# Kernel tuning notes

Hardware: AMD Instinct MI355X
Metric: run time of the kernel (lower is better)

Reference implementation:

```python
import jax, jax.numpy as jnp
import numpy as np

L, B, D, H = 2048, 2, 1024, 16
DK = D // H
SCALE = DK ** -0.5


def setup_inputs() -> dict:
    key = jax.random.key(0)
    ks = jax.random.split(key, 11)
    w_std = D ** -0.5
    return {
        "query": jax.random.normal(ks[0], (L, B, D), dtype=jnp.float32),
        "key": jax.random.normal(ks[1], (L, B, D), dtype=jnp.float32),
        "value": jax.random.normal(ks[2], (L, B, D), dtype=jnp.float32),
        "WQ_w": jax.random.normal(ks[3], (D, D), dtype=jnp.float32) * w_std,
        "WQ_b": jnp.zeros((D,), dtype=jnp.float32),
        "WK_w": jax.random.normal(ks[4], (D, D), dtype=jnp.float32) * w_std,
        "WK_b": jnp.zeros((D,), dtype=jnp.float32),
        "WV_w": jax.random.normal(ks[5], (D, D), dtype=jnp.float32) * w_std,
        "WV_b": jnp.zeros((D,), dtype=jnp.float32),
        "WO_w": jax.random.normal(ks[6], (D, D), dtype=jnp.float32) * w_std,
        "WO_b": jnp.zeros((D,), dtype=jnp.float32),
    }


def reference(query, key, value, WQ_w, WQ_b, WK_w, WK_b, WV_w, WV_b, WO_w, WO_b):
    tgt_len, batch, _ = query.shape
    src_len = key.shape[0]
    # linear projections (torch Linear: x @ W^T + b)
    q = (query @ WQ_w.T + WQ_b) * SCALE            # [L, B, D]
    k = key @ WK_w.T + WK_b                        # [S, B, D]
    v = value @ WV_w.T + WV_b                      # [S, B, D]
    # split heads: [len, B, D] -> [B*H, len, DK]
    q = q.reshape(tgt_len, batch * H, DK).transpose(1, 0, 2)
    k = k.reshape(src_len, batch * H, DK).transpose(1, 0, 2)
    v = v.reshape(src_len, batch * H, DK).transpose(1, 0, 2)
    # attention scores and softmax (full [B*H, L, S] matrix, as in the original)
    scores = jnp.einsum('nld,nsd->nls', q, k)      # [B*H, L, S]
    probs = jax.nn.softmax(scores, axis=-1)
    out = jnp.einsum('nls,nsd->nld', probs, v)     # [B*H, L, DK]
    # merge heads: [B*H, L, DK] -> [L, B, D]
    out = out.transpose(1, 0, 2).reshape(tgt_len, batch, D)
    return out @ WO_w.T + WO_b
```

## Files before the change

### kernel.cpp

```cpp
#include <hip/hip_runtime.h>
#include <hip/hip_fp16.h>

#define LL 2048
#define BB 2
#define DD 1024
#define HH 16
#define DKK 64

typedef _Float16 h8 __attribute__((ext_vector_type(8)));
typedef float f4 __attribute__((ext_vector_type(4)));
typedef float f16v __attribute__((ext_vector_type(16)));
typedef unsigned u2 __attribute__((ext_vector_type(2)));

#define BAR() do {                                              \
    asm volatile("s_waitcnt lgkmcnt(0)" ::: "memory");          \
    __builtin_amdgcn_s_barrier();                               \
    asm volatile("" ::: "memory");                              \
} while (0)

__device__ __forceinline__ void gload_lds16(const void* g, void* l) {
    __builtin_amdgcn_global_load_lds(
        (const __attribute__((address_space(1))) void*)g,
        (__attribute__((address_space(3))) void*)l, 16, 0, 0);
}

__device__ __forceinline__ unsigned pack2h(float a, float b) {
    union { __fp16 v __attribute__((ext_vector_type(2))); unsigned u; } x;
    x.v = __builtin_amdgcn_cvt_pkrtz(a, b);
    return x.u;
}

__device__ __forceinline__ size_t swz(int head, int l, int dk) {
    return ((((size_t)(head * 64 + (l >> 5)) * 4 + (dk >> 4)) * 2 +
             ((dk >> 3) & 1)) * 32 + (l & 31)) * 8 + (dk & 7);
}

__global__ __launch_bounds__(256) void cvt_w(
    const float* __restrict__ w0, const float* __restrict__ w1,
    const float* __restrict__ w2, const float* __restrict__ w3,
    _Float16* __restrict__ z0, _Float16* __restrict__ z1,
    _Float16* __restrict__ z2, _Float16* __restrict__ z3)
{
    const int sel = blockIdx.y;
    const float* src = (sel == 0) ? w0 : (sel == 1) ? w1 : (sel == 2) ? w2 : w3;
    _Float16* dst = (sel == 0) ? z0 : (sel == 1) ? z1 : (sel == 2) ? z2 : z3;
    const int i = (blockIdx.x * 256 + threadIdx.x) * 8;
    f4 a = *(const f4*)(src + i);
    f4 b = *(const f4*)(src + i + 4);
    h8 o = {(_Float16)a.x, (_Float16)a.y, (_Float16)a.z, (_Float16)a.w,
            (_Float16)b.x, (_Float16)b.y, (_Float16)b.z, (_Float16)b.w};
    *(h8*)(dst + i) = o;
}

__global__ __launch_bounds__(256) void qkv_proj(
    const float* __restrict__ xq, const float* __restrict__ xk,
    const float* __restrict__ xv,
    const _Float16* __restrict__ wq, const float* __restrict__ bq,
    const _Float16* __restrict__ wk, const float* __restrict__ bk,
    const _Float16* __restrict__ wv, const float* __restrict__ bv,
    _Float16* __restrict__ qhf, _Float16* __restrict__ khf,
    _Float16* __restrict__ vth)
{
    const int mode = blockIdx.z;
    const float*    X    = (mode == 0) ? xq : (mode == 1) ? xk : xv;
    const _Float16* W    = (mode == 0) ? wq : (mode == 1) ? wk : wv;
    const float*    bias = (mode == 0) ? bq : (mode == 1) ? bk : bv;

    __shared__ alignas(16) _Float16 a_sm[128 * 40];
    __shared__ alignas(16) _Float16 b_sm[128 * 32];

    const int tid  = threadIdx.x;
    const int lane = tid & 63;
    const int wave = tid >> 6;
    const int wm = (wave & 1) * 64;
    const int wn = (wave >> 1) * 64;
    const int m0 = blockIdx.x * 128;
    const int n0 = blockIdx.y * 128;

    const int srowA = tid >> 3;
    const int scolA = (tid & 7) * 4;
    const int srowB = tid >> 2;
    const int scolB = (tid & 3) * 8;
    const int ldsB  = wave * 512;

    f4 acc[4][4];
    #pragma unroll
    for (int i = 0; i < 4; i++)
        #pragma unroll
        for (int j = 0; j < 4; j++)
            #pragma unroll
            for (int r = 0; r < 4; r++) acc[i][j][r] = 0.f;

    const int fr = lane & 15;
    const int fk = (lane >> 4) * 8;

    for (int k0 = 0; k0 < DD; k0 += 32) {
        gload_lds16(W + (size_t)(n0 + srowB) * DD + k0 + scolB,      &b_sm[ldsB]);
        gload_lds16(W + (size_t)(n0 + 64 + srowB) * DD + k0 + scolB, &b_sm[2048 + ldsB]);
        #pragma unroll
        for (int r = 0; r < 4; r++) {
            f4 va = *(const f4*)(X + (size_t)(m0 + srowA + 32 * r) * DD + k0 + scolA);
            u2 pk = {pack2h(va.x, va.y), pack2h(va.z, va.w)};
            *(u2*)&a_sm[(srowA + 32 * r) * 40 + scolA] = pk;
        }
        __syncthreads();
        h8 af[4], bfr[4];
        #pragma unroll
        for (int i = 0; i < 4; i++) af[i]  = *(const h8*)&a_sm[(wm + i * 16 + fr) * 40 + fk];
        #pragma unroll
        for (int j = 0; j < 4; j++) bfr[j] = *(const h8*)&b_sm[(wn + j * 16 + fr) * 32 + fk];
        #pragma unroll
        for (int i = 0; i < 4; i++)
            #pragma unroll
            for (int j = 0; j < 4; j++)
                acc[i][j] = __builtin_amdgcn_mfma_f32_16x16x32_f16(af[i], bfr[j], acc[i][j], 0, 0, 0);
        __syncthreads();
    }

    const int colc = lane & 15;
    const int rowb = (lane >> 4) * 4;
    #pragma unroll
    for (int i = 0; i < 4; i++) {
        #pragma unroll
        for (int j = 0; j < 4; j++) {
            const int nn = n0 + wn + j * 16 + colc;
            const float bval = bias[nn];
            #pragma unroll
            for (int reg = 0; reg < 4; reg++) {
                const int mm = m0 + wm + i * 16 + rowb + reg;
                float v = acc[i][j][reg] + bval;
                const int b = mm & 1, l = mm >> 1;
                const int h = nn >> 6, dk = nn & 63;
                const int head = b * HH + h;
                if (mode == 0) {
                    v *= 0.1803368801111243f;
                    qhf[swz(head, l, dk)] = (_Float16)v;
                } else if (mode == 1) {
                    khf[swz(head, l, dk)] = (_Float16)v;
                } else {
                    vth[((size_t)head * DKK + dk) * LL + l] = (_Float16)v;
                }
            }
        }
    }
}

__global__ __launch_bounds__(256, 3) void attn(
    const _Float16* __restrict__ qhf, const _Float16* __restrict__ khf,
    const _Float16* __restrict__ vth, _Float16* __restrict__ oh)
{
    const int head = blockIdx.y;
    const int q0   = blockIdx.x * 64;
    const int tid = threadIdx.x, lane = tid & 63, wave = tid >> 6;
    const int qs = wave & 1;
    const int sw = wave >> 1;
    const int qw = q0 + qs * 32;

    __shared__ alignas(16) char smem[37376];
    _Float16* vtsm = (_Float16*)smem;

    const int rq = lane & 31;
    const int hi = lane >> 5;
    const int tid8 = tid * 8;

    const _Float16* vthead = vth + (size_t)head * DKK * LL;

    const _Float16* qbase = qhf + (size_t)(head * 64 + (qw >> 5)) * 2048;
    h8 qa[4];
    #pragma unroll
    for (int kf = 0; kf < 4; kf++)
        qa[kf] = *(const h8*)(qbase + kf * 512 + hi * 256 + rq * 8);

    const _Float16* kbase0 = khf + (size_t)(head * 64) * 2048;

    f16v o0, o1;
    #pragma unroll
    for (int r = 0; r < 16; r++) { o0[r] = 0.f; o1[r] = 0.f; }
    float lsum = 0.f;

    #pragma unroll
    for (int b2 = 0; b2 < 2; b2++)
        #pragma unroll
        for (int i = 0; i < 2; i++) {
            const int flat = i * 2048 + tid8;
            const int row = flat >> 6, col = flat & 63;
            *(h8*)&vtsm[b2 * 4608 + row * 72 + col] =
                *(const h8*)(vthead + (size_t)row * LL + b2 * 64 + col);
        }
    BAR();

    for (int it = 0; it < 16; ++it) {
        const int p = it & 1;
        const int s1 = it * 128 + 128;
        const bool more = (s1 < LL);

        const _Float16* kb = kbase0 + (size_t)(it * 4 + sw * 2) * 2048;
        h8 kc[2][4];
        #pragma unroll
        for (int st = 0; st < 2; st++)
            #pragma unroll
            for (int kf = 0; kf < 4; kf++)
                kc[st][kf] = *(const h8*)(kb + st * 2048 + kf * 512 + hi * 256 + rq * 8);

        h8 vpre[4];
        if (more) {
            #pragma unroll
            for (int b2 = 0; b2 < 2; b2++)
                #pragma unroll
                for (int i = 0; i < 2; i++) {
                    const int flat = i * 2048 + tid8;
                    const int row = flat >> 6, col = flat & 63;
                    vpre[b2 * 2 + i] =
                        *(const h8*)(vthead + (size_t)row * LL + s1 + b2 * 64 + col);
                }
        }

        const _Float16* vb = vtsm + p * 9216 + sw * 4608;

        #pragma unroll
        for (int st = 0; st < 2; st++) {
            f16v sc;
            #pragma unroll
            for (int r = 0; r < 16; r++) sc[r] = 0.f;
            #pragma unroll
            for (int kf = 0; kf < 4; kf++)
                sc = __builtin_amdgcn_mfma_f32_32x32x16_f16(kc[st][kf], qa[kf], sc, 0, 0, 0);

            float pr[16];
            #pragma unroll
            for (int r = 0; r < 16; r++) {
                pr[r] = __builtin_amdgcn_exp2f(sc[r]);
                lsum += pr[r];
            }
            unsigned own[4][2];
            #pragma unroll
            for (int g = 0; g < 4; g++) {
                own[g][0] = pack2h(pr[4 * g],     pr[4 * g + 1]);
                own[g][1] = pack2h(pr[4 * g + 2], pr[4 * g + 3]);
            }
            unsigned X0 = hi ? own[0][0] : own[1][0];
            unsigned X1 = hi ? own[0][1] : own[1][1];
            unsigned Y0 = hi ? own[2][0] : own[3][0];
            unsigned Y1 = hi ? own[2][1] : own[3][1];
            const unsigned rX0 = __shfl_xor(X0, 32, 64);
            const unsigned rX1 = __shfl_xor(X1, 32, 64);
            const unsigned rY0 = __shfl_xor(Y0, 32, 64);
            const unsigned rY1 = __shfl_xor(Y1, 32, 64);

            union { unsigned u[4]; h8 h; } pa0, pa1;
            pa0.u[0] = hi ? rX0 : own[0][0];
            pa0.u[1] = hi ? rX1 : own[0][1];
            pa0.u[2] = hi ? own[1][0] : rX0;
            pa0.u[3] = hi ? own[1][1] : rX1;
            pa1.u[0] = hi ? rY0 : own[2][0];
            pa1.u[1] = hi ? rY1 : own[2][1];
            pa1.u[2] = hi ? own[3][0] : rY0;
            pa1.u[3] = hi ? own[3][1] : rY1;

            const int vc0 = st * 32 + hi * 8;
            h8 b00 = *(const h8*)&vb[rq * 72 + vc0];
            h8 b10 = *(const h8*)&vb[(32 + rq) * 72 + vc0];
            o0 = __builtin_amdgcn_mfma_f32_32x32x16_f16(pa0.h, b00, o0, 0, 0, 0);
            o1 = __builtin_amdgcn_mfma_f32_32x32x16_f16(pa0.h, b10, o1, 0, 0, 0);
            h8 b01 = *(const h8*)&vb[rq * 72 + vc0 + 16];
            h8 b11 = *(const h8*)&vb[(32 + rq) * 72 + vc0 + 16];
            o0 = __builtin_amdgcn_mfma_f32_32x32x16_f16(pa1.h, b01, o0, 0, 0, 0);
            o1 = __builtin_amdgcn_mfma_f32_32x32x16_f16(pa1.h, b11, o1, 0, 0, 0);
        }

        if (more) {
            _Float16* wbuf = vtsm + (p ^ 1) * 9216;
            #pragma unroll
            for (int b2 = 0; b2 < 2; b2++)
                #pragma unroll
                for (int i = 0; i < 2; i++) {
                    const int flat = i * 2048 + tid8;
                    const int row = flat >> 6, col = flat & 63;
                    *(h8*)&wbuf[b2 * 4608 + row * 72 + col] = vpre[b2 * 2 + i];
                }
        }
        BAR();
    }

    lsum += __shfl_xor(lsum, 32, 64);

    float* comb = (float*)smem;
    float* lsp  = (float*)(smem + 36864);
    float* invp = (float*)(smem + 37120);

    if (wave >= 2) {
        float* c = comb + qs * 2048;
        #pragma unroll
        for (int r = 0; r < 16; r++) {
            const int row = (r & 3) + 8 * (r >> 2) + 4 * hi;
            c[row * 64 + rq]      = o0[r];
            c[row * 64 + 32 + rq] = o1[r];
        }
        if (hi == 0) lsp[qs * 32 + rq] = lsum;
    }
    BAR();
    if (wave < 2) {
        lsum += lsp[qs * 32 + rq];
        invp[qs * 32 + rq] = 1.0f / lsum;
        asm volatile("s_waitcnt lgkmcnt(0)" ::: "memory");
        const int b = head >> 4, h = head & 15;
        const float* c = comb + qs * 2048;
        #pragma unroll
        for (int r = 0; r < 16; r++) {
            const int row = (r & 3) + 8 * (r >> 2) + 4 * hi;
            const float inv = invp[qs * 32 + row];
            const int ql = qw + row;
            const size_t base = (size_t)(ql * BB + b) * DD + h * DKK;
            oh[base + rq]      = (_Float16)((o0[r] + c[row * 64 + rq]) * inv);
            oh[base + 32 + rq] = (_Float16)((o1[r] + c[row * 64 + 32 + rq]) * inv);
        }
    }
}

__global__ __launch_bounds__(256) void out_proj(
    const _Float16* __restrict__ oh, const _Float16* __restrict__ wo,
    const float* __restrict__ bo, float* __restrict__ out)
{
    __shared__ alignas(16) _Float16 a_sm[64 * 32];
    __shared__ alignas(16) _Float16 b_sm[128 * 32];
    const int tid = threadIdx.x, lane = tid & 63, wave = tid >> 6;
    const int wm = (wave & 1) * 32, wn = (wave >> 1) * 64;
    const int m0 = blockIdx.x * 64, n0 = blockIdx.y * 128;

    const int srow = tid >> 2;
    const int scol = (tid & 3) * 8;
    const int lds_base = wave * 512;

    f4 acc[2][4];
    #pragma unroll
    for (int i = 0; i < 2; i++)
        #pragma unroll
        for (int j = 0; j < 4; j++)
            #pragma unroll
            for (int r = 0; r < 4; r++) acc[i][j][r] = 0.f;

    const int fr = lane & 15;
    const int fk = (lane >> 4) * 8;

    for (int k0 = 0; k0 < DD; k0 += 32) {
        gload_lds16(oh + (size_t)(m0 + srow) * DD + k0 + scol,      &a_sm[lds_base]);
        gload_lds16(wo + (size_t)(n0 + srow) * DD + k0 + scol,      &b_sm[lds_base]);
        gload_lds16(wo + (size_t)(n0 + 64 + srow) * DD + k0 + scol, &b_sm[2048 + lds_base]);
        __syncthreads();
        h8 af[2], bfr[4];
        #pragma unroll
        for (int i = 0; i < 2; i++) af[i]  = *(const h8*)&a_sm[(wm + i * 16 + fr) * 32 + fk];
        #pragma unroll
        for (int j = 0; j < 4; j++) bfr[j] = *(const h8*)&b_sm[(wn + j * 16 + fr) * 32 + fk];
        #pragma unroll
        for (int i = 0; i < 2; i++)
            #pragma unroll
            for (int j = 0; j < 4; j++)
                acc[i][j] = __builtin_amdgcn_mfma_f32_16x16x32_f16(af[i], bfr[j], acc[i][j], 0, 0, 0);
        __syncthreads();
    }

    const int colc = lane & 15;
    const int rowb = (lane >> 4) * 4;
    #pragma unroll
    for (int i = 0; i < 2; i++) {
        #pragma unroll
        for (int j = 0; j < 4; j++) {
            const int nn = n0 + wn + j * 16 + colc;
            const float bval = bo[nn];
            #pragma unroll
            for (int reg = 0; reg < 4; reg++) {
                const int mm = m0 + wm + i * 16 + rowb + reg;
                out[(size_t)mm * DD + nn] = acc[i][j][reg] + bval;
            }
        }
    }
}

extern "C" void kernel_launch(void* const* d_in, const int* in_sizes, int n_in,
                              void* d_out, int out_size, void* d_ws, size_t ws_size,
                              hipStream_t stream) {
    const float* qin = (const float*)d_in[0];
    const float* kin = (const float*)d_in[1];
    const float* vin = (const float*)d_in[2];
    const float* wq  = (const float*)d_in[3];
    const float* bq  = (const float*)d_in[4];
    const float* wk  = (const float*)d_in[5];
    const float* bk  = (const float*)d_in[6];
    const float* wv  = (const float*)d_in[7];
    const float* bv  = (const float*)d_in[8];
    const float* wo  = (const float*)d_in[9];
    const float* bo  = (const float*)d_in[10];

    const size_t seg = (size_t)32 * LL * DKK;
    _Float16* qhf = (_Float16*)d_ws;
    _Float16* khf = qhf + seg;
    _Float16* vth = khf + seg;
    _Float16* oh  = vth + seg;
    _Float16* wqh = oh + seg;
    _Float16* wkh = wqh + (size_t)DD * DD;
    _Float16* wvh = wkh + (size_t)DD * DD;
    _Float16* woh = wvh + (size_t)DD * DD;

    hipLaunchKernelGGL(cvt_w, dim3(512, 4), dim3(256), 0, stream,
                       wq, wk, wv, wo, wqh, wkh, wvh, woh);
    hipLaunchKernelGGL(qkv_proj, dim3(32, 8, 3), dim3(256), 0, stream,
                       qin, kin, vin, wqh, bq, wkh, bk, wvh, bv, qhf, khf, vth);
    hipLaunchKernelGGL(attn, dim3(32, 32), dim3(256), 0, stream, qhf, khf, vth, oh);
    hipLaunchKernelGGL(out_proj, dim3(64, 8), dim3(256), 0, stream, oh, woh,
                       bo, (float*)d_out);
}
```

Measured before the change: 267.8 us.

## Pre-convert activations to fp16, load via LDS DMA, use row-major Q/K with prefetch

Extends the conversion kernel so the three input activations are also cast to fp16 up front. The QKV projection can then stream both operands with global_load_lds instead of converting fp32 in registers. Q and K are now stored plain row-major per head instead of in the swizzled MFMA-fragment layout. The attention kernel prefetches the next K block into registers one iteration ahead. This adds a full extra read and write pass over the activations, and the row-major K loads are strided rather than contiguous.

```diff
diff --git a/kernel.cpp b/kernel.cpp
--- a/kernel.cpp
+++ b/kernel.cpp
@@ -10,7 +10,6 @@
 typedef _Float16 h8 __attribute__((ext_vector_type(8)));
 typedef float f4 __attribute__((ext_vector_type(4)));
 typedef float f16v __attribute__((ext_vector_type(16)));
-typedef unsigned u2 __attribute__((ext_vector_type(2)));
 
 #define BAR() do {                                              \
     asm volatile("s_waitcnt lgkmcnt(0)" ::: "memory");          \
@@ -30,20 +29,22 @@
     return x.u;
 }
 
-__device__ __forceinline__ size_t swz(int head, int l, int dk) {
-    return ((((size_t)(head * 64 + (l >> 5)) * 4 + (dk >> 4)) * 2 +
-             ((dk >> 3) & 1)) * 32 + (l & 31)) * 8 + (dk & 7);
-}
-
-__global__ __launch_bounds__(256) void cvt_w(
-    const float* __restrict__ w0, const float* __restrict__ w1,
-    const float* __restrict__ w2, const float* __restrict__ w3,
-    _Float16* __restrict__ z0, _Float16* __restrict__ z1,
-    _Float16* __restrict__ z2, _Float16* __restrict__ z3)
+__global__ __launch_bounds__(256) void cvt_all(
+    const float* __restrict__ x0, const float* __restrict__ x1,
+    const float* __restrict__ x2, const float* __restrict__ w0,
+    const float* __restrict__ w1, const float* __restrict__ w2,
+    const float* __restrict__ w3,
+    _Float16* __restrict__ y0, _Float16* __restrict__ y1,
+    _Float16* __restrict__ y2, _Float16* __restrict__ z0,
+    _Float16* __restrict__ z1, _Float16* __restrict__ z2,
+    _Float16* __restrict__ z3)
 {
     const int sel = blockIdx.y;
-    const float* src = (sel == 0) ? w0 : (sel == 1) ? w1 : (sel == 2) ? w2 : w3;
-    _Float16* dst = (sel == 0) ? z0 : (sel == 1) ? z1 : (sel == 2) ? z2 : z3;
+    if (sel >= 3 && blockIdx.x >= 512) return;
+    const float* src = (sel == 0) ? x0 : (sel == 1) ? x1 : (sel == 2) ? x2
+                     : (sel == 3) ? w0 : (sel == 4) ? w1 : (sel == 5) ? w2 : w3;
+    _Float16* dst = (sel == 0) ? y0 : (sel == 1) ? y1 : (sel == 2) ? y2
+                  : (sel == 3) ? z0 : (sel == 4) ? z1 : (sel == 5) ? z2 : z3;
     const int i = (blockIdx.x * 256 + threadIdx.x) * 8;
     f4 a = *(const f4*)(src + i);
     f4 b = *(const f4*)(src + i + 4);
@@ -53,20 +54,20 @@
 }
 
 __global__ __launch_bounds__(256) void qkv_proj(
-    const float* __restrict__ xq, const float* __restrict__ xk,
-    const float* __restrict__ xv,
+    const _Float16* __restrict__ xq, const _Float16* __restrict__ xk,
+    const _Float16* __restrict__ xv,
     const _Float16* __restrict__ wq, const float* __restrict__ bq,
     const _Float16* __restrict__ wk, const float* __restrict__ bk,
     const _Float16* __restrict__ wv, const float* __restrict__ bv,
-    _Float16* __restrict__ qhf, _Float16* __restrict__ khf,
+    _Float16* __restrict__ qh, _Float16* __restrict__ kh,
     _Float16* __restrict__ vth)
 {
     const int mode = blockIdx.z;
-    const float*    X    = (mode == 0) ? xq : (mode == 1) ? xk : xv;
+    const _Float16* X    = (mode == 0) ? xq : (mode == 1) ? xk : xv;
     const _Float16* W    = (mode == 0) ? wq : (mode == 1) ? wk : wv;
     const float*    bias = (mode == 0) ? bq : (mode == 1) ? bk : bv;
 
-    __shared__ alignas(16) _Float16 a_sm[128 * 40];
+    __shared__ alignas(16) _Float16 a_sm[128 * 32];
     __shared__ alignas(16) _Float16 b_sm[128 * 32];
 
     const int tid  = threadIdx.x;
@@ -77,11 +78,9 @@
     const int m0 = blockIdx.x * 128;
     const int n0 = blockIdx.y * 128;
 
-    const int srowA = tid >> 3;
-    const int scolA = (tid & 7) * 4;
-    const int srowB = tid >> 2;
-    const int scolB = (tid & 3) * 8;
-    const int ldsB  = wave * 512;
+    const int srow = tid >> 2;
+    const int scol = (tid & 3) * 8;
+    const int lds_base = wave * 512;
 
     f4 acc[4][4];
     #pragma unroll
@@ -95,18 +94,14 @@
     const int fk = (lane >> 4) * 8;
 
     for (int k0 = 0; k0 < DD; k0 += 32) {
-        gload_lds16(W + (size_t)(n0 + srowB) * DD + k0 + scolB,      &b_sm[ldsB]);
-        gload_lds16(W + (size_t)(n0 + 64 + srowB) * DD + k0 + scolB, &b_sm[2048 + ldsB]);
-        #pragma unroll
-        for (int r = 0; r < 4; r++) {
-            f4 va = *(const f4*)(X + (size_t)(m0 + srowA + 32 * r) * DD + k0 + scolA);
-            u2 pk = {pack2h(va.x, va.y), pack2h(va.z, va.w)};
-            *(u2*)&a_sm[(srowA + 32 * r) * 40 + scolA] = pk;
-        }
+        gload_lds16(X + (size_t)(m0 + srow) * DD + k0 + scol,       &a_sm[lds_base]);
+        gload_lds16(X + (size_t)(m0 + 64 + srow) * DD + k0 + scol,  &a_sm[2048 + lds_base]);
+        gload_lds16(W + (size_t)(n0 + srow) * DD + k0 + scol,       &b_sm[lds_base]);
+        gload_lds16(W + (size_t)(n0 + 64 + srow) * DD + k0 + scol,  &b_sm[2048 + lds_base]);
         __syncthreads();
         h8 af[4], bfr[4];
         #pragma unroll
-        for (int i = 0; i < 4; i++) af[i]  = *(const h8*)&a_sm[(wm + i * 16 + fr) * 40 + fk];
+        for (int i = 0; i < 4; i++) af[i]  = *(const h8*)&a_sm[(wm + i * 16 + fr) * 32 + fk];
         #pragma unroll
         for (int j = 0; j < 4; j++) bfr[j] = *(const h8*)&b_sm[(wn + j * 16 + fr) * 32 + fk];
         #pragma unroll
@@ -134,9 +129,9 @@
                 const int head = b * HH + h;
                 if (mode == 0) {
                     v *= 0.1803368801111243f;
-                    qhf[swz(head, l, dk)] = (_Float16)v;
+                    qh[((size_t)head * LL + l) * DKK + dk] = (_Float16)v;
                 } else if (mode == 1) {
-                    khf[swz(head, l, dk)] = (_Float16)v;
+                    kh[((size_t)head * LL + l) * DKK + dk] = (_Float16)v;
                 } else {
                     vth[((size_t)head * DKK + dk) * LL + l] = (_Float16)v;
                 }
@@ -146,7 +141,7 @@
 }
 
 __global__ __launch_bounds__(256, 3) void attn(
-    const _Float16* __restrict__ qhf, const _Float16* __restrict__ khf,
+    const _Float16* __restrict__ qh, const _Float16* __restrict__ kh,
     const _Float16* __restrict__ vth, _Float16* __restrict__ oh)
 {
     const int head = blockIdx.y;
@@ -163,15 +158,22 @@
     const int hi = lane >> 5;
     const int tid8 = tid * 8;
 
+    const _Float16* khead  = kh  + (size_t)head * LL * DKK;
     const _Float16* vthead = vth + (size_t)head * DKK * LL;
 
-    const _Float16* qbase = qhf + (size_t)(head * 64 + (qw >> 5)) * 2048;
+    const _Float16* qbase = qh + ((size_t)head * LL + qw + rq) * DKK;
     h8 qa[4];
     #pragma unroll
     for (int kf = 0; kf < 4; kf++)
-        qa[kf] = *(const h8*)(qbase + kf * 512 + hi * 256 + rq * 8);
-
-    const _Float16* kbase0 = khf + (size_t)(head * 64) * 2048;
+        qa[kf] = *(const h8*)(qbase + kf * 16 + hi * 8);
+
+    h8 kc[2][4];
+    #pragma unroll
+    for (int st = 0; st < 2; st++)
+        #pragma unroll
+        for (int kf = 0; kf < 4; kf++)
+            kc[st][kf] = *(const h8*)(khead +
+                (size_t)(sw * 64 + st * 32 + rq) * DKK + kf * 16 + hi * 8);
 
     f16v o0, o1;
     #pragma unroll
@@ -194,16 +196,14 @@
         const int s1 = it * 128 + 128;
         const bool more = (s1 < LL);
 
-        const _Float16* kb = kbase0 + (size_t)(it * 4 + sw * 2) * 2048;
-        h8 kc[2][4];
-        #pragma unroll
-        for (int st = 0; st < 2; st++)
-            #pragma unroll
-            for (int kf = 0; kf < 4; kf++)
-                kc[st][kf] = *(const h8*)(kb + st * 2048 + kf * 512 + hi * 256 + rq * 8);
-
-        h8 vpre[4];
+        h8 kpre[2][4], vpre[4];
         if (more) {
+            #pragma unroll
+            for (int st = 0; st < 2; st++)
+                #pragma unroll
+                for (int kf = 0; kf < 4; kf++)
+                    kpre[st][kf] = *(const h8*)(khead +
+                        (size_t)(s1 + sw * 64 + st * 32 + rq) * DKK + kf * 16 + hi * 8);
             #pragma unroll
             for (int b2 = 0; b2 < 2; b2++)
                 #pragma unroll
@@ -278,6 +278,11 @@
                     const int row = flat >> 6, col = flat & 63;
                     *(h8*)&wbuf[b2 * 4608 + row * 72 + col] = vpre[b2 * 2 + i];
                 }
+            #pragma unroll
+            for (int st = 0; st < 2; st++)
+                #pragma unroll
+                for (int kf = 0; kf < 4; kf++)
+                    kc[st][kf] = kpre[st][kf];
         }
         BAR();
     }
@@ -393,20 +398,24 @@
     const float* bo  = (const float*)d_in[10];
 
     const size_t seg = (size_t)32 * LL * DKK;
-    _Float16* qhf = (_Float16*)d_ws;
-    _Float16* khf = qhf + seg;
-    _Float16* vth = khf + seg;
+    _Float16* qh  = (_Float16*)d_ws;
+    _Float16* kh  = qh + seg;
+    _Float16* vth = kh + seg;
     _Float16* oh  = vth + seg;
     _Float16* wqh = oh + seg;
     _Float16* wkh = wqh + (size_t)DD * DD;
     _Float16* wvh = wkh + (size_t)DD * DD;
     _Float16* woh = wvh + (size_t)DD * DD;
-
-    hipLaunchKernelGGL(cvt_w, dim3(512, 4), dim3(256), 0, stream,
-                       wq, wk, wv, wo, wqh, wkh, wvh, woh);
+    _Float16* xqh = woh + (size_t)DD * DD;
+    _Float16* xkh = xqh + seg;
+    _Float16* xvh = xkh + seg;
+
+    hipLaunchKernelGGL(cvt_all, dim3(2048, 7), dim3(256), 0, stream,
+                       qin, kin, vin, wq, wk, wv, wo,
+                       xqh, xkh, xvh, wqh, wkh, wvh, woh);
     hipLaunchKernelGGL(qkv_proj, dim3(32, 8, 3), dim3(256), 0, stream,
-                       qin, kin, vin, wqh, bq, wkh, bk, wvh, bv, qhf, khf, vth);
-    hipLaunchKernelGGL(attn, dim3(32, 32), dim3(256), 0, stream, qhf, khf, vth, oh);
+                       xqh, xkh, xvh, wqh, bq, wkh, bk, wvh, bv, qh, kh, vth);
+    hipLaunchKernelGGL(attn, dim3(32, 32), dim3(256), 0, stream, qh, kh, vth, oh);
     hipLaunchKernelGGL(out_proj, dim3(64, 8), dim3(256), 0, stream, oh, woh,
                        bo, (float*)d_out);
 }
```

Result: faster. 253.1 us (-5.5%).
